# Kernel optimization log

Measured on AMD Instinct MI355X. Metric: run time of the kernel, lower is better.

Reference implementation:

```python
import jax, jax.numpy as jnp
import numpy as np

B, T, N, CIN, C, L, NC, S = 8, 64, 200, 200, 128, 2, 2, 100
SPARSITY = 30


def bn(x, g, b, eps=1e-5):
    # BatchNorm1d forward with batch statistics (training-mode math, biased var)
    m = x.mean(0)
    v = x.var(0)
    return (x - m) / jnp.sqrt(v + eps) * g + b


def ln(x, g, b, eps=1e-5):
    m = x.mean(-1, keepdims=True)
    v = x.var(-1, keepdims=True)
    return (x - m) / jnp.sqrt(v + eps) * g + b


def setup_inputs() -> dict:
    key = jax.random.key(0)
    ks = iter(jax.random.split(key, 64))

    def nrm(shape, s=0.02):
        return jax.random.normal(next(ks), shape, jnp.float32) * s

    return dict(
        fMRI_v=jax.random.normal(next(ks), (B, T, N, CIN), jnp.float32),
        fMRI_a=jax.random.uniform(next(ks), (B, T, N, N), jnp.float32),
        sMRI_trad=jax.random.normal(next(ks), (B, S), jnp.float32),
        sMRI_deep=jnp.zeros((B, 1, 8, 8, 8), jnp.float32),
        csatt=1, CA_MOD=0,
        w_init=nrm((CIN, C)), b_init=jnp.zeros((C,), jnp.float32),
        gin_eps=jnp.zeros((L,), jnp.float32),
        gin_w1=nrm((L, C, C)), gin_b1=jnp.zeros((L, C), jnp.float32),
        gin_bn1_g=jnp.ones((L, C), jnp.float32), gin_bn1_b=jnp.zeros((L, C), jnp.float32),
        gin_w2=nrm((L, C, C)), gin_b2=jnp.zeros((L, C), jnp.float32),
        gin_bn2_g=jnp.ones((L, C), jnp.float32), gin_bn2_b=jnp.zeros((L, C), jnp.float32),
        sero_w=nrm((L, C, C)), sero_b=jnp.zeros((L, C), jnp.float32),
        sero_bn_g=jnp.ones((L, C), jnp.float32), sero_bn_b=jnp.zeros((L, C), jnp.float32),
        sero_aw=nrm((L, C, N)), sero_ab=jnp.zeros((L, N), jnp.float32),
        tr_wqkv=nrm((L, C, 3 * C)), tr_bqkv=jnp.zeros((L, 3 * C), jnp.float32),
        tr_wo=nrm((L, C, C)), tr_bo=jnp.zeros((L, C), jnp.float32),
        tr_ln1_g=jnp.ones((L, C), jnp.float32), tr_ln1_b=jnp.zeros((L, C), jnp.float32),
        tr_ln2_g=jnp.ones((L, C), jnp.float32), tr_ln2_b=jnp.zeros((L, C), jnp.float32),
        tr_w1=nrm((L, C, 2 * C)), tr_b1=jnp.zeros((L, 2 * C), jnp.float32),
        tr_w2=nrm((L, 2 * C, C)), tr_b2=jnp.zeros((L, C), jnp.float32),
        cls_w=nrm((L, C, NC)), cls_b=jnp.zeros((L, NC), jnp.float32),
        smri_w=nrm((S, C)), smri_b=jnp.zeros((C,), jnp.float32),
        smri_bn_g=jnp.ones((C,), jnp.float32), smri_bn_b=jnp.zeros((C,), jnp.float32),
    )


def reference(fMRI_v, fMRI_a, sMRI_trad, sMRI_deep, csatt, CA_MOD,
              w_init, b_init, gin_eps,
              gin_w1, gin_b1, gin_bn1_g, gin_bn1_b,
              gin_w2, gin_b2, gin_bn2_g, gin_bn2_b,
              sero_w, sero_b, sero_bn_g, sero_bn_b, sero_aw, sero_ab,
              tr_wqkv, tr_bqkv, tr_wo, tr_bo,
              tr_ln1_g, tr_ln1_b, tr_ln2_g, tr_ln2_b,
              tr_w1, tr_b1, tr_w2, tr_b2,
              cls_w, cls_b, smri_w, smri_b, smri_bn_g, smri_bn_b):
    b, t, n = fMRI_a.shape[:3]
    # initial linear over flattened (b t n) tokens
    h3 = (fMRI_v.reshape(-1, fMRI_v.shape[-1]) @ w_init + b_init).reshape(b, t, n, -1)
    # _collate_adjacency: per-(sample,timepoint) percentile threshold -> block-diag sparse
    # with all-ones values; equivalent to a batched masked matmul.
    thr = jnp.percentile(fMRI_a, 100 - SPARSITY, axis=(-2, -1), keepdims=True)
    mask = (fMRI_a > thr).astype(h3.dtype)  # [b,t,n,n]

    logit = jnp.zeros((b, cls_w.shape[-1]), h3.dtype)
    latents, node_attns, time_attns = [], [], []
    scale = 1.0 / jnp.sqrt(jnp.asarray(h3.shape[-1], h3.dtype))
    for l in range(L):
        # LayerGIN: note the original feeds h3 (initial features) to EVERY layer
        agg = jnp.einsum('btij,btjc->btic', mask, h3) + gin_eps[l] * h3
        x = agg.reshape(-1, agg.shape[-1])
        x = jax.nn.relu(bn(x @ gin_w1[l] + gin_b1[l], gin_bn1_g[l], gin_bn1_b[l]))
        x = jax.nn.relu(bn(x @ gin_w2[l] + gin_b2[l], gin_bn2_g[l], gin_bn2_b[l]))
        hb = x.reshape(b, t, n, -1).transpose(1, 0, 2, 3)  # (t,b,n,c)
        # ModuleSERO readout (node_axis=2)
        xr = hb.mean(2)  # (t,b,c)
        e = jax.nn.gelu(bn(xr.reshape(t * b, -1) @ sero_w[l] + sero_b[l],
                           sero_bn_g[l], sero_bn_b[l]), approximate=False)
        ga = jax.nn.sigmoid(e @ sero_aw[l] + sero_ab[l]).reshape(t, b, n)
        hr = (hb * ga[..., None]).mean(2)  # (t,b,c)
        node_attns.append(ga.transpose(1, 0, 2))  # (b,t,n)
        # ModuleTransformer (single head, post-LN, no residual before ln1)
        qkv = hr @ tr_wqkv[l] + tr_bqkv[l]
        q, k, v = jnp.split(qkv, 3, axis=-1)
        A = jax.nn.softmax(jnp.einsum('tbc,sbc->bts', q, k) * scale, axis=-1)  # (b,t,t)
        att = jnp.einsum('bts,sbc->tbc', A, v) @ tr_wo[l] + tr_bo[l]
        x1 = ln(att, tr_ln1_g[l], tr_ln1_b[l])
        m = jax.nn.relu(x1 @ tr_w1[l] + tr_b1[l]) @ tr_w2[l] + tr_b2[l]
        x2 = ln(x1 + m, tr_ln2_g[l], tr_ln2_b[l])
        time_attns.append(A)
        lat = x2.sum(0)  # cls_token='sum' over time
        logit = logit + lat @ cls_w[l] + cls_b[l]
        latents.append(lat)
    feat_fMRI = jnp.stack(latents, 1).mean(1)  # (b,c)
    feat_sMRI = bn(sMRI_trad @ smri_w + smri_b, smri_bn_g, smri_bn_b)
    node_attn = jnp.stack(node_attns, 1)  # (b,L,t,n)
    time_attn = jnp.stack(time_attns, 1)  # (b,L,t,t)
    return (logit, feat_fMRI, feat_sMRI, node_attn, time_attn)
```

## Files before the change

### kernel.cpp

```cpp
#include <hip/hip_runtime.h>
#include <math.h>

#define B_   8
#define T_   64
#define N_   200
#define CIN_ 200
#define C_   128
#define L_   2
#define NC_  2
#define S_   100
#define BT_  512
#define RB_  102400

#define ACT_NONE 0
#define ACT_RELU 1
#define ACT_GELU 2

typedef __attribute__((ext_vector_type(8))) short short8v;
typedef __attribute__((ext_vector_type(4))) float f32x4v;

union U4S8 { uint4 u; short8v s; };

__device__ __forceinline__ unsigned short f2bf(float f) {
    unsigned u = __float_as_uint(f);
    unsigned r = (u + 0x7FFFu + ((u >> 16) & 1u)) >> 16;
    return (unsigned short)r;
}
__device__ __forceinline__ float bf2f(unsigned short u) {
    return __uint_as_float(((unsigned)u) << 16);
}
__device__ __forceinline__ float bflo(unsigned u) { return __uint_as_float(u << 16); }
__device__ __forceinline__ float bfhi(unsigned u) { return __uint_as_float(u & 0xFFFF0000u); }
__device__ __forceinline__ unsigned packbf(float a, float b) {
    return (unsigned)f2bf(a) | ((unsigned)f2bf(b) << 16);
}

#define GLL(src, dst) __builtin_amdgcn_global_load_lds( \
    (const __attribute__((address_space(1))) unsigned int*)(src), \
    (__attribute__((address_space(3))) unsigned int*)(dst), 16, 0, 0)

__global__ __launch_bounds__(1024) void thr_kernel(const float* __restrict__ a,
                                                   float* __restrict__ thr,
                                                   unsigned* __restrict__ msk) {
    __shared__ int      hist[1024];
    __shared__ int      red[1024];
    __shared__ unsigned smask[1400];
    __shared__ float    candV[6144];
    __shared__ unsigned short candP[6144];
    __shared__ int      part[256];
    __shared__ int      grp[32];
    __shared__ float    cand2[256];
    __shared__ int      meta[8];
    __shared__ float    s_thr;
    int tid = threadIdx.x, lane = tid & 63;
    int bt = blockIdx.x;
    hist[tid] = 0;
    for (int i = tid; i < 1400; i += 1024) smask[i] = 0u;
    if (tid == 0) { meta[0] = 0; meta[1] = 0; }
    __syncthreads();

    const float4* x4 = (const float4*)(a + (long)bt * 40000);
    int c_lo = 0;
    #pragma unroll 1
    for (int it = 0; it < 10; it++) {
        int i4 = tid + it * 1024;
        unsigned nhi = 0u, ncm = 0u;
        float vv[4] = {0.f, 0.f, 0.f, 0.f};
        if (i4 < 10000) {
            float4 v = x4[i4];
            vv[0] = v.x; vv[1] = v.y; vv[2] = v.z; vv[3] = v.w;
            #pragma unroll
            for (int j = 0; j < 4; j++) {
                float f = vv[j];
                if (f < 0.65f) c_lo++;
                else if (f < 0.75f) ncm |= 1u << j;
                else nhi |= 1u << j;
            }
            if (nhi) {
                int vi = i4 * 4;
                int row = vi / 200, col = vi - row * 200;
                atomicOr(&smask[row * 7 + (col >> 5)], nhi << (col & 31));
            }
        }
        int cnt = __popc(ncm);
        int pfx = cnt;
        #pragma unroll
        for (int d = 1; d < 64; d <<= 1) {
            int t = __shfl_up(pfx, d, 64);
            if (lane >= d) pfx += t;
        }
        int total = __shfl(pfx, 63, 64);
        if (total) {
            int bw = 0;
            if (lane == 63) bw = atomicAdd(&meta[0], total);
            bw = __shfl(bw, 63, 64);
            int p = bw + pfx - cnt;
            #pragma unroll
            for (int j = 0; j < 4; j++) {
                if ((ncm >> j) & 1u) {
                    float f = vv[j];
                    if (p < 6144) { candV[p] = f; candP[p] = (unsigned short)(i4 * 4 + j); }
                    int bin = (int)((f - 0.65f) * 10240.0f);
                    bin = bin < 0 ? 0 : (bin > 1023 ? 1023 : bin);
                    atomicAdd(&hist[bin], 1);
                    p++;
                }
            }
        }
    }
    red[tid] = c_lo;
    __syncthreads();
    for (int off = 512; off; off >>= 1) {
        if (tid < off) red[tid] += red[tid + off];
        __syncthreads();
    }
    int c_lo_tot = red[0];
    if (tid < 256) part[tid] = hist[4*tid] + hist[4*tid+1] + hist[4*tid+2] + hist[4*tid+3];
    __syncthreads();
    if (tid < 32) {
        int s = 0;
        for (int i = 0; i < 8; i++) s += part[8*tid + i];
        grp[tid] = s;
    }
    __syncthreads();
    if (tid == 0) {
        int r = 27999 - c_lo_tot;
        int cum = 0, g = 0;
        while (cum + grp[g] <= r) cum += grp[g++];
        int t = g * 8;
        while (cum + part[t] <= r) cum += part[t++];
        int b = t * 4;
        while (cum + hist[b] <= r) cum += hist[b++];
        meta[2] = b; meta[3] = cum;
        int r1 = r + 1;
        cum = 0; g = 0;
        while (cum + grp[g] <= r1) cum += grp[g++];
        t = g * 8;
        while (cum + part[t] <= r1) cum += part[t++];
        b = t * 4;
        while (cum + hist[b] <= r1) cum += hist[b++];
        meta[4] = b; meta[5] = r;
    }
    __syncthreads();
    int blo = meta[2], base = meta[3], bhi = meta[4], r = meta[5];
    int m = meta[0]; if (m > 6144) m = 6144;
    for (int i = tid; i < m; i += 1024) {
        float v = candV[i];
        int bin = (int)((v - 0.65f) * 10240.0f);
        bin = bin < 0 ? 0 : (bin > 1023 ? 1023 : bin);
        if (bin >= blo && bin <= bhi) {
            int p = atomicAdd(&meta[1], 1);
            if (p < 256) cand2[p] = v;
        }
    }
    __syncthreads();
    if (tid == 0) {
        int m2 = meta[1]; if (m2 > 256) m2 = 256;
        for (int i = 1; i < m2; i++) {
            float key = cand2[i]; int j = i - 1;
            while (j >= 0 && cand2[j] > key) { cand2[j+1] = cand2[j]; j--; }
            cand2[j+1] = key;
        }
        float s1 = cand2[r - base], s2 = cand2[r + 1 - base];
        float tv = s1 * 0.701171875f + s2 * 0.298828125f;
        thr[bt] = tv;
        s_thr = tv;
    }
    __syncthreads();
    float tv = s_thr;
    for (int i = tid; i < m; i += 1024) {
        if (candV[i] > tv) {
            int vi = candP[i];
            int row = vi / 200, col = vi - row * 200;
            atomicOr(&smask[row * 7 + (col >> 5)], 1u << (col & 31));
        }
    }
    __syncthreads();
    for (int i = tid; i < 1400; i += 1024)
        msk[(long)bt * 1400 + i] = smask[i];
}

__global__ void wtcvt_kernel(const float* __restrict__ w, int K, int Kpad,
                             unsigned short* __restrict__ wt) {
    int c = blockIdx.x;
    for (int k = threadIdx.x; k < Kpad; k += 64) {
        float v = (k < K) ? w[(long)k * 128 + c] : 0.f;
        wt[(long)c * Kpad + k] = f2bf(v);
    }
}

template<bool A_BF16, bool BN_IN, bool BIAS_OUT, bool STATS_OUT>
__global__ __launch_bounds__(256) void gemm_direct_kernel(
        const void* __restrict__ xv, int K, int Kstride, int Ksteps,
        const unsigned short* __restrict__ wt, int Kpad,
        const float* __restrict__ bias, const float* __restrict__ statsIn,
        const float* __restrict__ bng, const float* __restrict__ bnb,
        unsigned short* __restrict__ y, float* __restrict__ statsOut) {
    constexpr int ASZ  = A_BF16 ? 8192 : 16384;
    constexpr int BOFF = 2 * ASZ;
    constexpr int NEED = 2 * ASZ + 2 * 8192;
    constexpr int POOL = NEED > 32768 ? NEED : 32768;
    __shared__ unsigned char pool[POOL];
    __shared__ float bnS[128], bnB[128];
    int tid = threadIdx.x;
    if (BN_IN) {
        if (tid < 128) {
            float mm = statsIn[tid] * (1.f / (float)RB_);
            float var = fmaxf(statsIn[128 + tid] * (1.f / (float)RB_) - mm * mm, 0.f);
            float sc = bng[tid] / sqrtf(var + 1e-5f);
            bnS[tid] = sc; bnB[tid] = bnb[tid] - mm * sc;
        }
    }
    int wave = tid >> 6, lane = tid & 63, quad = lane >> 4, m16 = lane & 15;
    long row0g = (long)blockIdx.x * 128;

    auto STAGE = [&](int buf, int ks) {
        #pragma unroll
        for (int j = 0; j < 2; j++) {
            int r = j * 64 + (tid >> 2);
            int c = (tid & 3) ^ ((r >> 1) & 3);
            const char* src = (const char*)wt + (long)r * (Kpad * 2) + ks * 64 + c * 16;
            char* dst = (char*)pool + BOFF + buf * 8192 + j * 4096 + wave * 1024;
            GLL(src, dst);
        }
        if (A_BF16) {
            const char* xb = (const char*)xv;
            #pragma unroll
            for (int j = 0; j < 2; j++) {
                int r = j * 64 + (tid >> 2);
                int c = (tid & 3) ^ ((r >> 1) & 3);
                const char* src = xb + ((row0g + r) * Kstride + ks * 32) * 2 + c * 16;
                char* dst = (char*)pool + buf * ASZ + j * 4096 + wave * 1024;
                GLL(src, dst);
            }
        } else {
            const char* xb = (const char*)xv;
            #pragma unroll
            for (int j = 0; j < 4; j++) {
                int r = j * 32 + (tid >> 3);
                int c = (tid & 7) ^ (r & 7);
                const char* src = xb + ((row0g + r) * Kstride + ks * 32) * 4 + c * 16;
                char* dst = (char*)pool + buf * ASZ + j * 4096 + wave * 1024;
                GLL(src, dst);
            }
        }
    };

    f32x4v acc[2][8];
    #pragma unroll
    for (int i = 0; i < 2; i++)
        #pragma unroll
        for (int j = 0; j < 8; j++) acc[i][j] = (f32x4v){0.f, 0.f, 0.f, 0.f};

    STAGE(0, 0);
    __syncthreads();

    for (int ks = 0; ks < Ksteps; ks++) {
        if (ks + 1 < Ksteps) {
            STAGE((ks + 1) & 1, ks + 1);
            if (A_BF16) asm volatile("s_waitcnt vmcnt(4)" ::: "memory");
            else        asm volatile("s_waitcnt vmcnt(6)" ::: "memory");
        } else {
            asm volatile("s_waitcnt vmcnt(0)" ::: "memory");
        }
        __builtin_amdgcn_s_barrier();
        asm volatile("" ::: "memory");

        const char* Ab = (const char*)pool + (ks & 1) * ASZ;
        const char* Bb = (const char*)pool + BOFF + (ks & 1) * 8192;
        int kf = ks * 32 + quad * 8;
        U4S8 bU[8];
        #pragma unroll
        for (int nt = 0; nt < 8; nt++) {
            int r = nt * 16 + m16;
            int ch = quad ^ ((r >> 1) & 3);
            bU[nt].u = *(const uint4*)(Bb + r * 64 + ch * 16);
        }
        U4S8 aU[2];
        if (A_BF16) {
            #pragma unroll
            for (int mt = 0; mt < 2; mt++) {
                int r = wave * 32 + mt * 16 + m16;
                int ch = quad ^ ((r >> 1) & 3);
                aU[mt].u = *(const uint4*)(Ab + r * 64 + ch * 16);
            }
            if (BN_IN) {
                float4 s0 = *(const float4*)&bnS[kf], s1 = *(const float4*)&bnS[kf + 4];
                float4 b0 = *(const float4*)&bnB[kf], b1 = *(const float4*)&bnB[kf + 4];
                #pragma unroll
                for (int mt = 0; mt < 2; mt++) {
                    uint4 u = aU[mt].u;
                    float f0 = fmaxf(bflo(u.x) * s0.x + b0.x, 0.f);
                    float f1 = fmaxf(bfhi(u.x) * s0.y + b0.y, 0.f);
                    float f2 = fmaxf(bflo(u.y) * s0.z + b0.z, 0.f);
                    float f3 = fmaxf(bfhi(u.y) * s0.w + b0.w, 0.f);
                    float f4 = fmaxf(bflo(u.z) * s1.x + b1.x, 0.f);
                    float f5 = fmaxf(bfhi(u.z) * s1.y + b1.y, 0.f);
                    float f6 = fmaxf(bflo(u.w) * s1.z + b1.z, 0.f);
                    float f7 = fmaxf(bfhi(u.w) * s1.w + b1.w, 0.f);
                    u.x = packbf(f0, f1); u.y = packbf(f2, f3);
                    u.z = packbf(f4, f5); u.w = packbf(f6, f7);
                    aU[mt].u = u;
                }
            }
        } else {
            #pragma unroll
            for (int mt = 0; mt < 2; mt++) {
                int r = wave * 32 + mt * 16 + m16;
                int swz = r & 7;
                const char* base = Ab + r * 128;
                float4 v0 = *(const float4*)(base + ((2 * quad) ^ swz) * 16);
                float4 v1 = *(const float4*)(base + ((2 * quad + 1) ^ swz) * 16);
                uint4 o;
                o.x = packbf(v0.x, v0.y); o.y = packbf(v0.z, v0.w);
                o.z = packbf(v1.x, v1.y); o.w = packbf(v1.z, v1.w);
                aU[mt].u = o;
            }
        }
        #pragma unroll
        for (int nt = 0; nt < 8; nt++) {
            acc[0][nt] = __builtin_amdgcn_mfma_f32_16x16x32_bf16(aU[0].s, bU[nt].s, acc[0][nt], 0, 0, 0);
            acc[1][nt] = __builtin_amdgcn_mfma_f32_16x16x32_bf16(aU[1].s, bU[nt].s, acc[1][nt], 0, 0, 0);
        }
        asm volatile("s_waitcnt lgkmcnt(0)" ::: "memory");
        __builtin_amdgcn_s_barrier();
        asm volatile("" ::: "memory");
    }
    if (!A_BF16 && (K & 31) != 0) {
        int kf = Ksteps * 32 + quad * 8;
        U4S8 bU[8];
        #pragma unroll
        for (int nt = 0; nt < 8; nt++)
            bU[nt].u = *(const uint4*)&wt[(long)(nt * 16 + m16) * Kpad + kf];
        U4S8 aU[2];
        const float* x = (const float*)xv;
        #pragma unroll
        for (int mt = 0; mt < 2; mt++) {
            uint4 o = {0u, 0u, 0u, 0u};
            if (kf + 8 <= K) {
                const float* p = &x[(row0g + wave * 32 + mt * 16 + m16) * Kstride + kf];
                float4 v0 = *(const float4*)p;
// ... 251 lines not shown
    unsigned ONEu = 0x3F80u;

    f32x4v acc[2][8];
    #pragma unroll
    for (int i = 0; i < 2; i++)
        #pragma unroll
        for (int j = 0; j < 8; j++) acc[i][j] = (f32x4v){0.f, 0.f, 0.f, 0.f};

    __syncthreads();

    for (int kc = 0; kc < 7; kc++) {
        if (kc < 4) STAGE((kc + 3) & 3, kc + 3);
        if (kc == 3)      asm volatile("s_waitcnt vmcnt(6)" ::: "memory");
        else if (kc == 4) asm volatile("s_waitcnt vmcnt(4)" ::: "memory");
        else if (kc == 5) asm volatile("s_waitcnt vmcnt(2)" ::: "memory");
        else if (kc == 6) asm volatile("s_waitcnt vmcnt(0)" ::: "memory");
        __builtin_amdgcn_s_barrier();
        asm volatile("" ::: "memory");

        const char* sb = (const char*)&u.stage[kc & 3][0];
        U4S8 bU[8];
        #pragma unroll
        for (int nt = 0; nt < 8; nt++) {
            int r = nt * 16 + m16;
            int q = quad ^ ((r >> 1) & 3);
            bU[nt].u = *(const uint4*)(sb + r * 64 + q * 16);
        }
        U4S8 aU[2];
        #pragma unroll
        for (int mt = 0; mt < 2; mt++) {
            int lr = wave * 32 + mt * 16 + m16;
            unsigned bits = (sbits[lr * 7 + kc] >> (quad * 8)) & 0xFFu;
            unsigned o[4];
            #pragma unroll
            for (int p = 0; p < 4; p++) {
                unsigned lo = ((bits >> (2 * p)) & 1u) ? ONEu : 0u;
                unsigned hi = ((bits >> (2 * p + 1)) & 1u) ? ONEu : 0u;
                o[p] = lo | (hi << 16);
            }
            aU[mt].u = make_uint4(o[0], o[1], o[2], o[3]);
        }
        #pragma unroll
        for (int nt = 0; nt < 8; nt++) {
            acc[0][nt] = __builtin_amdgcn_mfma_f32_16x16x32_bf16(aU[0].s, bU[nt].s, acc[0][nt], 0, 0, 0);
            acc[1][nt] = __builtin_amdgcn_mfma_f32_16x16x32_bf16(aU[1].s, bU[nt].s, acc[1][nt], 0, 0, 0);
        }
        asm volatile("s_waitcnt lgkmcnt(0)" ::: "memory");
        __builtin_amdgcn_s_barrier();
        asm volatile("" ::: "memory");
    }

    #pragma unroll
    for (int nt = 0; nt < 8; nt++) {
        int col = nt * 16 + m16;
        #pragma unroll
        for (int mt = 0; mt < 2; mt++) {
            int lrb = wave * 32 + mt * 16 + quad * 4;
            #pragma unroll
            for (int i = 0; i < 4; i++) {
                int lr = lrb + i;
                u.trans[lr * 128 + (col ^ ((lr & 6) << 2))] = f2bf(acc[mt][nt][i]);
            }
        }
    }
    __syncthreads();

    float eps = geps[l];
    f32x4v acc2[2][8];
    #pragma unroll
    for (int i = 0; i < 2; i++)
        #pragma unroll
        for (int j = 0; j < 8; j++) acc2[i][j] = (f32x4v){0.f, 0.f, 0.f, 0.f};

    for (int ks = 0; ks < 4; ks++) {
        int kf = ks * 32 + quad * 8;
        U4S8 bU[8];
        #pragma unroll
        for (int nt = 0; nt < 8; nt++)
            bU[nt].u = *(const uint4*)&w1t[(long)(nt * 16 + m16) * 128 + kf];
        U4S8 aU[2];
        #pragma unroll
        for (int mt = 0; mt < 2; mt++) {
            int r = wave * 32 + mt * 16 + m16;
            uint4 mu = *(const uint4*)&u.trans[r * 128 + (kf ^ ((r & 6) << 2))];
            int gr = row0 + r;
            uint4 hu = {0u, 0u, 0u, 0u};
            if (gr < N_) hu = *(const uint4*)&h3[((long)bt * N_ + gr) * 128 + kf];
            float f0 = bflo(mu.x) + eps * bflo(hu.x);
            float f1 = bfhi(mu.x) + eps * bfhi(hu.x);
            float f2 = bflo(mu.y) + eps * bflo(hu.y);
            float f3 = bfhi(mu.y) + eps * bfhi(hu.y);
            float f4 = bflo(mu.z) + eps * bflo(hu.z);
            float f5 = bfhi(mu.z) + eps * bfhi(hu.z);
            float f6 = bflo(mu.w) + eps * bflo(hu.w);
            float f7 = bfhi(mu.w) + eps * bfhi(hu.w);
            uint4 o;
            o.x = packbf(f0, f1); o.y = packbf(f2, f3);
            o.z = packbf(f4, f5); o.w = packbf(f6, f7);
            aU[mt].u = o;
        }
        #pragma unroll
        for (int nt = 0; nt < 8; nt++) {
            acc2[0][nt] = __builtin_amdgcn_mfma_f32_16x16x32_bf16(aU[0].s, bU[nt].s, acc2[0][nt], 0, 0, 0);
            acc2[1][nt] = __builtin_amdgcn_mfma_f32_16x16x32_bf16(aU[1].s, bU[nt].s, acc2[1][nt], 0, 0, 0);
        }
    }
    __syncthreads();

    float sAcc[8], qAcc[8];
    #pragma unroll
    for (int nt = 0; nt < 8; nt++) {
        int col = nt * 16 + m16;
        float bv = b1[col];
        float s = 0.f, q = 0.f;
        #pragma unroll
        for (int mt = 0; mt < 2; mt++) {
            int lrb = wave * 32 + mt * 16 + quad * 4;
            #pragma unroll
            for (int i = 0; i < 4; i++) {
                int lr = lrb + i;
                float v = acc2[mt][nt][i] + bv;
                u.trans[lr * 128 + (col ^ ((lr & 6) << 2))] = f2bf(v);
                if (row0 + lr < N_) { s += v; q += v * v; }
            }
        }
        sAcc[nt] = s; qAcc[nt] = q;
    }
    __syncthreads();
    #pragma unroll
    for (int rnd = 0; rnd < 8; rnd++) {
        int row = rnd * 16 + (tid >> 4), ch = tid & 15;
        int gr = row0 + row;
        uint4 v = *(const uint4*)&u.trans[row * 128 + ((ch * 8) ^ ((row & 6) << 2))];
        if (gr < N_)
            *(uint4*)&y[((long)bt * N_ + gr) * 128 + ch * 8] = v;
    }
    __syncthreads();
    #pragma unroll
    for (int nt = 0; nt < 8; nt++) {
        int col = nt * 16 + m16;
        u.red.S[col * 16 + wave * 4 + quad] = sAcc[nt];
        u.red.Q[col * 16 + wave * 4 + quad] = qAcc[nt];
    }
    __syncthreads();
    if (tid < 128) {
        float s = 0.f, q = 0.f;
        #pragma unroll
        for (int j = 0; j < 16; j++) { s += u.red.S[tid * 16 + j]; q += u.red.Q[tid * 16 + j]; }
        atomicAdd(&statsOut[tid], s);
        atomicAdd(&statsOut[128 + tid], q);
    }
}

__global__ __launch_bounds__(256) void xr2_kernel(const unsigned short* __restrict__ raw,
                                                  const float* __restrict__ stats,
                                                  const float* __restrict__ g,
                                                  const float* __restrict__ b,
                                                  float* __restrict__ xr) {
    __shared__ float red[256];
    int tid = threadIdx.x, c = tid & 127, hf = tid >> 7;
    int t = blockIdx.x / B_, bb = blockIdx.x % B_;
    const unsigned short* base = raw + ((long)bb * T_ + t) * N_ * C_;
    float m = stats[c] * (1.f / (float)RB_);
    float var = fmaxf(stats[128 + c] * (1.f / (float)RB_) - m * m, 0.f);
    float sc = g[c] / sqrtf(var + 1e-5f);
    float sh = b[c] - m * sc;
    float s = 0.f;
    for (int n = hf * 100; n < hf * 100 + 100; n++)
        s += fmaxf(fmaf(bf2f(base[n * C_ + c]), sc, sh), 0.f);
    red[tid] = s;
    __syncthreads();
    if (hf == 0)
        xr[(long)blockIdx.x * C_ + c] = (red[c] + red[c + 128]) * (1.f / 200.f);
}

__global__ __launch_bounds__(256) void hr2_kernel(const unsigned short* __restrict__ raw,
                                                  const float* __restrict__ stats,
                                                  const float* __restrict__ g,
                                                  const float* __restrict__ b,
                                                  const float* __restrict__ ga,
                                                  float* __restrict__ hr) {
    __shared__ float sga[N_];
    __shared__ float red[256];
    int tid = threadIdx.x, c = tid & 127, hf = tid >> 7;
    int t = blockIdx.x / B_, bb = blockIdx.x % B_;
    const unsigned short* base = raw + ((long)bb * T_ + t) * N_ * C_;
    for (int i = tid; i < N_; i += 256) sga[i] = ga[(long)blockIdx.x * N_ + i];
    __syncthreads();
    float m = stats[c] * (1.f / (float)RB_);
    float var = fmaxf(stats[128 + c] * (1.f / (float)RB_) - m * m, 0.f);
    float sc = g[c] / sqrtf(var + 1e-5f);
    float sh = b[c] - m * sc;
    float s = 0.f;
    for (int n = hf * 100; n < hf * 100 + 100; n++)
        s = fmaf(fmaxf(fmaf(bf2f(base[n * C_ + c]), sc, sh), 0.f), sga[n], s);
    red[tid] = s;
    __syncthreads();
    if (hf == 0)
        hr[(long)blockIdx.x * C_ + c] = (red[c] + red[c + 128]) * (1.f / 200.f);
}

template<int K, int ROWS, bool STATS>
__global__ void mm_kernel(const float* __restrict__ x, const float* __restrict__ w,
                          const float* __restrict__ bias, float* __restrict__ y,
                          int Cout, int act, float* __restrict__ stats) {
    __shared__ float sx[ROWS * K];
    long r0 = (long)blockIdx.x * ROWS;
    for (int idx = threadIdx.x; idx < ROWS * K; idx += blockDim.x)
        sx[idx] = x[r0 * K + idx];
    __syncthreads();
    int c = threadIdx.x;
    float acc[ROWS];
    #pragma unroll
    for (int i = 0; i < ROWS; i++) acc[i] = 0.f;
    for (int k = 0; k < K; k++) {
        float wv = w[k * Cout + c];
        #pragma unroll
        for (int i = 0; i < ROWS; i++) acc[i] = fmaf(sx[i * K + k], wv, acc[i]);
    }
    float bv = bias ? bias[c] : 0.f;
    float s = 0.f, ss = 0.f;
    for (int i = 0; i < ROWS; i++) {
        float vv = acc[i] + bv;
        if (act == ACT_RELU) vv = fmaxf(vv, 0.f);
        y[(r0 + i) * Cout + c] = vv;
        if (STATS) { s += vv; ss += vv * vv; }
    }
    if (STATS) {
        atomicAdd(&stats[c], s);
        atomicAdd(&stats[C_ + c], ss);
    }
}

__global__ __launch_bounds__(256) void ga_kernel(const float* __restrict__ eRaw,
                          const float* __restrict__ stats,
                          const float* __restrict__ sg, const float* __restrict__ sb,
                          const float* __restrict__ aw, const float* __restrict__ ab,
                          float* __restrict__ ga, float* __restrict__ node_out, int l) {
    __shared__ float sx[4 * C_];
    __shared__ float bnS[C_], bnB[C_];
    int tid = threadIdx.x;
    if (tid < C_) {
        float m = stats[tid] * (1.f / (float)BT_);
        float var = fmaxf(stats[C_ + tid] * (1.f / (float)BT_) - m * m, 0.f);
        float inv = 1.f / sqrtf(var + 1e-5f);
        float sc = inv * sg[tid];
        bnS[tid] = sc;
        bnB[tid] = sb[tid] - m * sc;
    }
    __syncthreads();
    long r0 = (long)blockIdx.x * 4;
    for (int idx = tid; idx < 4 * C_; idx += 256) {
        int col = idx & (C_ - 1);
        float v = eRaw[r0 * C_ + idx] * bnS[col] + bnB[col];
        sx[idx] = 0.5f * v * (1.f + erff(v * 0.70710678118654752f));
    }
    __syncthreads();
    int c = tid;
    if (c < N_) {
        float acc[4] = {0.f, 0.f, 0.f, 0.f};
        for (int k = 0; k < C_; k++) {
            float wv = aw[k * N_ + c];
            #pragma unroll
            for (int i = 0; i < 4; i++) acc[i] = fmaf(sx[i * C_ + k], wv, acc[i]);
        }
        float bv = ab[c];
        for (int i = 0; i < 4; i++) {
            int tb = (int)r0 + i;
            int t = tb / B_, b = tb % B_;
            float v = 1.f / (1.f + expf(-(acc[i] + bv)));
            ga[(long)tb * N_ + c] = v;
            node_out[(((long)b * L_ + l) * T_ + t) * N_ + c] = v;
        }
    }
}

__global__ __launch_bounds__(128) void attnav_kernel(const float* __restrict__ qkv,
                            float* __restrict__ time_out, float* __restrict__ attv, int l) {
    __shared__ float q[C_];
    __shared__ float sa[T_];
    int tid = threadIdx.x;
    int t = blockIdx.x / B_, b = blockIdx.x % B_;
    q[tid] = qkv[((long)t * B_ + b) * 384 + tid];
    __syncthreads();
    if (tid < 64) {
        const float* krow = qkv + ((long)tid * B_ + b) * 384 + C_;
        float s = 0.f;
        for (int c = 0; c < C_; c++) s = fmaf(q[c], krow[c], s);
        s *= 0.08838834764831843f;
        float mx = s;
        #pragma unroll
        for (int off = 32; off; off >>= 1) mx = fmaxf(mx, __shfl_xor(mx, off));
        float e = expf(s - mx), sum = e;
        #pragma unroll
        for (int off = 32; off; off >>= 1) sum += __shfl_xor(sum, off);
        float p = e / sum;
        sa[tid] = p;
        time_out[(((long)b * L_ + l) * T_ + t) * T_ + tid] = p;
    }
    __syncthreads();
    float s2 = 0.f;
    for (int sp = 0; sp < T_; sp++)
        s2 = fmaf(sa[sp], qkv[((long)sp * B_ + b) * 384 + 256 + tid], s2);
    attv[((long)t * B_ + b) * C_ + tid] = s2;
}

__global__ __launch_bounds__(128) void mmln_kernel(const float* __restrict__ x,
                          const float* __restrict__ w, const float* __restrict__ bias,
                          const float* __restrict__ g, const float* __restrict__ bb,
                          float* __restrict__ out) {
    __shared__ float sx[2 * C_];
    __shared__ float red[C_];
    int tid = threadIdx.x;
    long r0 = (long)blockIdx.x * 2;
    sx[tid]       = x[r0 * C_ + tid];
    sx[C_ + tid]  = x[r0 * C_ + C_ + tid];
    __syncthreads();
    float a0 = 0.f, a1 = 0.f;
    for (int k = 0; k < C_; k++) {
        float wv = w[k * C_ + tid];
        a0 = fmaf(sx[k], wv, a0);
        a1 = fmaf(sx[C_ + k], wv, a1);
    }
    float bv = bias[tid];
    float v[2] = {a0 + bv, a1 + bv};
    #pragma unroll 1
    for (int r = 0; r < 2; r++) {
        red[tid] = v[r]; __syncthreads();
        for (int off = 64; off; off >>= 1) { if (tid < off) red[tid] += red[tid + off]; __syncthreads(); }
        float m = red[0] * (1.f / C_); __syncthreads();
        float d = v[r] - m;
        red[tid] = d * d; __syncthreads();
        for (int off = 64; off; off >>= 1) { if (tid < off) red[tid] += red[tid + off]; __syncthreads(); }
        float var = red[0] * (1.f / C_); __syncthreads();
        out[(r0 + r) * C_ + tid] = d * (1.f / sqrtf(var + 1e-5f)) * g[tid] + bb[tid];
    }
}

__global__ __launch_bounds__(256) void ffn_kernel(const float* __restrict__ x1,
                          const float* __restrict__ w1, const float* __restrict__ b1,
                          const float* __restrict__ w2, const float* __restrict__ b2,
                          const float* __restrict__ g, const float* __restrict__ bb,
                          float* __restrict__ out) {
    __shared__ float sx[2 * C_];
    __shared__ float mid[2 * 256];
    __shared__ float red[C_];
    int tid = threadIdx.x;
    long r0 = (long)blockIdx.x * 2;
    sx[tid] = x1[r0 * C_ + tid];
    __syncthreads();
    float a0 = 0.f, a1 = 0.f;
    for (int k = 0; k < C_; k++) {
        float wv = w1[k * 256 + tid];
        a0 = fmaf(sx[k], wv, a0);
        a1 = fmaf(sx[C_ + k], wv, a1);
    }
    float bv = b1[tid];
    mid[tid]       = fmaxf(a0 + bv, 0.f);
    mid[256 + tid] = fmaxf(a1 + bv, 0.f);
    __syncthreads();
    float v[2] = {0.f, 0.f};
    if (tid < C_) {
        float c0 = 0.f, c1 = 0.f;
        for (int k = 0; k < 256; k++) {
            float wv = w2[k * C_ + tid];
            c0 = fmaf(mid[k], wv, c0);
            c1 = fmaf(mid[256 + k], wv, c1);
        }
        float bv2 = b2[tid];
        v[0] = c0 + bv2 + sx[tid];
        v[1] = c1 + bv2 + sx[C_ + tid];
    }
    #pragma unroll 1
    for (int r = 0; r < 2; r++) {
        if (tid < C_) red[tid] = v[r];
        __syncthreads();
        for (int off = 64; off; off >>= 1) { if (tid < off) red[tid] += red[tid + off]; __syncthreads(); }
        float m = red[0] * (1.f / C_); __syncthreads();
        float d = v[r] - m;
        if (tid < C_) red[tid] = d * d;
        __syncthreads();
        for (int off = 64; off; off >>= 1) { if (tid < off) red[tid] += red[tid + off]; __syncthreads(); }
        float var = red[0] * (1.f / C_); __syncthreads();
        if (tid < C_)
            out[(r0 + r) * C_ + tid] = d * (1.f / sqrtf(var + 1e-5f)) * g[tid] + bb[tid];
    }
}

__global__ void latsum_kernel(const float* __restrict__ x2, float* __restrict__ lat) {
    int b = blockIdx.x, c = threadIdx.x;
    float s = 0.f;
    for (int t = 0; t < T_; t++) s += x2[((long)t * B_ + b) * C_ + c];
    lat[(long)b * C_ + c] = s;
}

__global__ void final_kernel(const float* __restrict__ lat, const float* __restrict__ cls_w,
                             const float* __restrict__ cls_b, float* __restrict__ out) {
    int idx = blockIdx.x * blockDim.x + threadIdx.x;
    if (idx < B_ * NC_) {
        int b = idx / NC_, nc = idx % NC_;
        float s = 0.f;
        for (int l = 0; l < L_; l++) {
            float acc = 0.f;
            for (int c = 0; c < C_; c++)
                acc = fmaf(lat[l * B_ * C_ + b * C_ + c], cls_w[l * C_ * NC_ + c * NC_ + nc], acc);
            s += acc + cls_b[l * NC_ + nc];
        }
        out[idx] = s;
    } else if (idx < B_ * NC_ + B_ * C_) {
        int j = idx - B_ * NC_;
        out[idx] = 0.5f * (lat[j] + lat[B_ * C_ + j]);
    }
}

__global__ void smri_kernel(const float* __restrict__ trad, const float* __restrict__ w,
                            const float* __restrict__ bias, const float* __restrict__ g,
                            const float* __restrict__ bb, float* __restrict__ out) {
    int c = threadIdx.x;
    float y[B_];
    for (int b = 0; b < B_; b++) {
        float s = bias[c];
        for (int k = 0; k < S_; k++) s = fmaf(trad[b * S_ + k], w[k * C_ + c], s);
        y[b] = s;
    }
    float m = 0.f;
    for (int b = 0; b < B_; b++) m += y[b];
    m *= (1.f / B_);
    float var = 0.f;
    for (int b = 0; b < B_; b++) { float d = y[b] - m; var += d * d; }
    var *= (1.f / B_);
    float inv = 1.f / sqrtf(var + 1e-5f);
    for (int b = 0; b < B_; b++) out[b * C_ + c] = (y[b] - m) * inv * g[c] + bb[c];
}

extern "C" void kernel_launch(void* const* d_in, const int* in_sizes, int n_in,
                              void* d_out, int out_size, void* d_ws, size_t ws_size,
                              hipStream_t stream) {
    const float* fv       = (const float*)d_in[0];
    const float* fa       = (const float*)d_in[1];
    const float* trad     = (const float*)d_in[2];
    const float* w_init   = (const float*)d_in[6];
    const float* b_init   = (const float*)d_in[7];
    const float* gin_eps  = (const float*)d_in[8];
    const float* gin_w1   = (const float*)d_in[9];
    const float* gin_b1   = (const float*)d_in[10];
    const float* gbn1g    = (const float*)d_in[11];
    const float* gbn1b    = (const float*)d_in[12];
    const float* gin_w2   = (const float*)d_in[13];
    const float* gin_b2   = (const float*)d_in[14];
    const float* gbn2g    = (const float*)d_in[15];
    const float* gbn2b    = (const float*)d_in[16];
    const float* sero_w   = (const float*)d_in[17];
    const float* sero_b   = (const float*)d_in[18];
    const float* sbng     = (const float*)d_in[19];
    const float* sbnb     = (const float*)d_in[20];
    const float* sero_aw  = (const float*)d_in[21];
    const float* sero_ab  = (const float*)d_in[22];
    const float* wqkv     = (const float*)d_in[23];
    const float* bqkv     = (const float*)d_in[24];
    const float* wo       = (const float*)d_in[25];
    const float* bo       = (const float*)d_in[26];
    const float* ln1g     = (const float*)d_in[27];
    const float* ln1b     = (const float*)d_in[28];
    const float* ln2g     = (const float*)d_in[29];
    const float* ln2b     = (const float*)d_in[30];
    const float* tw1      = (const float*)d_in[31];
    const float* tb1      = (const float*)d_in[32];
    const float* tw2      = (const float*)d_in[33];
    const float* tb2      = (const float*)d_in[34];
    const float* cls_w    = (const float*)d_in[35];
    const float* cls_b    = (const float*)d_in[36];
    const float* smri_w   = (const float*)d_in[37];
    const float* smri_b   = (const float*)d_in[38];
    const float* smri_g   = (const float*)d_in[39];
    const float* smri_bb  = (const float*)d_in[40];

    float* out = (float*)d_out;

    const long SZ_BIG = (long)RB_ * C_;
    unsigned short* H3b = (unsigned short*)d_ws;
    unsigned short* Y1b = H3b + SZ_BIG;
    unsigned short* Y2b = Y1b + SZ_BIG;
    unsigned short* ZTb = Y2b + SZ_BIG;
    float* fbase = (float*)(ZTb + (long)BT_ * 128 * 224);
    float* THR  = fbase;
    float* STAT = THR + 512;
    float* XR   = STAT + 256;
    float* E    = XR  + BT_ * C_;
    float* GA   = E   + BT_ * C_;
    float* HR   = GA  + BT_ * N_;
    float* QKV  = HR  + BT_ * C_;
    float* ATTV = QKV + BT_ * 3 * C_;
    float* ATT  = ATTV + BT_ * C_;
    float* X1   = ATT + BT_ * C_;
    float* MMB  = X1  + BT_ * C_;
    float* X2   = MMB + BT_ * 2 * C_;
    float* LAT  = X2  + BT_ * C_;
    float* STATB = MMB;
    unsigned short* WT0 = (unsigned short*)(LAT + L_ * B_ * C_);
    unsigned short* WT1 = WT0 + 128 * 224;
    unsigned short* WT2 = WT1 + 2 * 128 * 128;
    unsigned* MSK = (unsigned*)(WT2 + 2 * 128 * 128);

    float* OUT_LOGIT = out;
    float* OUT_FEATS = out + 1040;
    float* OUT_NODE  = out + 2064;
    float* OUT_TIME  = out + 206864;

    wtcvt_kernel<<<128, 64, 0, stream>>>(w_init, 200, 224, WT0);
    wtcvt_kernel<<<128, 64, 0, stream>>>(gin_w1,           128, 128, WT1);
    wtcvt_kernel<<<128, 64, 0, stream>>>(gin_w1 + C_ * C_, 128, 128, WT1 + 128 * 128);
    wtcvt_kernel<<<128, 64, 0, stream>>>(gin_w2,           128, 128, WT2);
    wtcvt_kernel<<<128, 64, 0, stream>>>(gin_w2 + C_ * C_, 128, 128, WT2 + 128 * 128);

    h3gemmT_kernel<<<RB_ / 128, 256, 0, stream>>>(fv, WT0, b_init, H3b, ZTb);
    thr_kernel<<<BT_, 1024, 0, stream>>>(fa, THR, MSK);

    for (int l = 0; l < L_; l++) {
        hipMemsetAsync(STAT, 0, 256 * sizeof(float), stream);
        maskfused_kernel<<<BT_ * 2, 256, 0, stream>>>(MSK, ZTb, H3b, WT1 + l * 128 * 128,
            gin_eps, l, gin_b1 + l * C_, Y2b, STAT);
        hipMemsetAsync(STATB, 0, 256 * sizeof(float), stream);
        gemm_direct_kernel<true, true, true, true><<<RB_ / 128, 256, 0, stream>>>(
            Y2b, 128, 128, 4, WT2 + l * 128 * 128, 128, gin_b2 + l * C_, STAT,
            gbn1g + l * C_, gbn1b + l * C_, Y1b, STATB);
        xr2_kernel<<<BT_, 256, 0, stream>>>(Y1b, STATB, gbn2g + l * C_, gbn2b + l * C_, XR);

        hipMemsetAsync(STAT, 0, 256 * sizeof(float), stream);
        mm_kernel<128, 2, true><<<BT_ / 2, 128, 0, stream>>>(
            XR, sero_w + l * C_ * C_, sero_b + l * C_, E, C_, ACT_NONE, STAT);
        ga_kernel<<<BT_ / 4, 256, 0, stream>>>(E, STAT, sbng + l * C_, sbnb + l * C_,
            sero_aw + l * C_ * N_, sero_ab + l * N_, GA, OUT_NODE, l);
        hr2_kernel<<<BT_, 256, 0, stream>>>(Y1b, STATB, gbn2g + l * C_, gbn2b + l * C_, GA, HR);

        mm_kernel<128, 2, false><<<BT_ / 2, 384, 0, stream>>>(
            HR, wqkv + l * C_ * 3 * C_, bqkv + l * 3 * C_, QKV, 3 * C_, ACT_NONE, nullptr);
        attnav_kernel<<<BT_, 128, 0, stream>>>(QKV, OUT_TIME, ATTV, l);
        mmln_kernel<<<BT_ / 2, 128, 0, stream>>>(ATTV, wo + l * C_ * C_, bo + l * C_,
            ln1g + l * C_, ln1b + l * C_, X1);
        ffn_kernel<<<BT_ / 2, 256, 0, stream>>>(X1, tw1 + l * C_ * 2 * C_, tb1 + l * 2 * C_,
            tw2 + l * 2 * C_ * C_, tb2 + l * C_, ln2g + l * C_, ln2b + l * C_, X2);
        latsum_kernel<<<B_, 128, 0, stream>>>(X2, LAT + l * B_ * C_);
    }

    final_kernel<<<5, 256, 0, stream>>>(LAT, cls_w, cls_b, OUT_LOGIT);
    smri_kernel<<<1, 128, 0, stream>>>(trad, smri_w, smri_b, smri_g, smri_bb, OUT_FEATS);
}
```

Before: 773.6 us.

## Fuse small tail kernels and batch weight conversion and memsets

Merges the five weight-conversion launches into one kernel and replaces the per-layer stat memsets with a single upfront memset over per-layer stat buffers. Fuses the node-mean reduction with the SERO linear layer, the weighted node-mean with the QKV projection, the attention with the output projection and LayerNorm, and the FFN output with the time-sum via atomics. This cuts launch count and intermediate global traffic in the latency-bound tail. In exchange, some fused matvecs now run with less parallelism per block, and the atomic time-sum gives a nondeterministic summation order.

```diff
diff --git a/kernel.cpp b/kernel.cpp
--- a/kernel.cpp
+++ b/kernel.cpp
@@ -11,10 +11,6 @@
 #define S_   100
 #define BT_  512
 #define RB_  102400
-
-#define ACT_NONE 0
-#define ACT_RELU 1
-#define ACT_GELU 2
 
 typedef __attribute__((ext_vector_type(8))) short short8v;
 typedef __attribute__((ext_vector_type(4))) float f32x4v;
@@ -180,13 +176,19 @@
         msk[(long)bt * 1400 + i] = smask[i];
 }
 
-__global__ void wtcvt_kernel(const float* __restrict__ w, int K, int Kpad,
-                             unsigned short* __restrict__ wt) {
-    int c = blockIdx.x;
-    for (int k = threadIdx.x; k < Kpad; k += 64) {
-        float v = (k < K) ? w[(long)k * 128 + c] : 0.f;
-        wt[(long)c * Kpad + k] = f2bf(v);
-    }
+__global__ void wtcvt5_kernel(const float* __restrict__ w_init,
+                              const float* __restrict__ gin_w1,
+                              const float* __restrict__ gin_w2,
+                              unsigned short* __restrict__ WT0,
+                              unsigned short* __restrict__ WT1,
+                              unsigned short* __restrict__ WT2) {
+    int grp = blockIdx.x >> 7, c = blockIdx.x & 127;
+    const float* w; unsigned short* wt; int K, Kpad;
+    if (grp == 0)      { w = w_init;                     wt = WT0;                     K = 200; Kpad = 224; }
+    else if (grp <= 2) { w = gin_w1 + (grp - 1) * C_ * C_; wt = WT1 + (grp - 1) * 128 * 128; K = 128; Kpad = 128; }
+    else               { w = gin_w2 + (grp - 3) * C_ * C_; wt = WT2 + (grp - 3) * 128 * 128; K = 128; Kpad = 128; }
+    for (int k = threadIdx.x; k < Kpad; k += 64)
+        wt[(long)c * Kpad + k] = f2bf((k < K) ? w[(long)k * 128 + c] : 0.f);
 }
 
 template<bool A_BF16, bool BN_IN, bool BIAS_OUT, bool STATS_OUT>
@@ -744,12 +746,13 @@
     }
 }
 
-__global__ __launch_bounds__(256) void xr2_kernel(const unsigned short* __restrict__ raw,
-                                                  const float* __restrict__ stats,
-                                                  const float* __restrict__ g,
-                                                  const float* __restrict__ b,
-                                                  float* __restrict__ xr) {
+__global__ __launch_bounds__(256) void xrE_kernel(
+        const unsigned short* __restrict__ raw, const float* __restrict__ stats,
+        const float* __restrict__ g, const float* __restrict__ b,
+        const float* __restrict__ sw, const float* __restrict__ sb,
+        float* __restrict__ E, float* __restrict__ statE) {
     __shared__ float red[256];
+    __shared__ float xrrow[128];
     int tid = threadIdx.x, c = tid & 127, hf = tid >> 7;
     int t = blockIdx.x / B_, bb = blockIdx.x % B_;
     const unsigned short* base = raw + ((long)bb * T_ + t) * N_ * C_;
@@ -762,65 +765,18 @@
         s += fmaxf(fmaf(bf2f(base[n * C_ + c]), sc, sh), 0.f);
     red[tid] = s;
     __syncthreads();
-    if (hf == 0)
-        xr[(long)blockIdx.x * C_ + c] = (red[c] + red[c + 128]) * (1.f / 200.f);
-}
-
-__global__ __launch_bounds__(256) void hr2_kernel(const unsigned short* __restrict__ raw,
-                                                  const float* __restrict__ stats,
-                                                  const float* __restrict__ g,
-                                                  const float* __restrict__ b,
-                                                  const float* __restrict__ ga,
-                                                  float* __restrict__ hr) {
-    __shared__ float sga[N_];
-    __shared__ float red[256];
-    int tid = threadIdx.x, c = tid & 127, hf = tid >> 7;
-    int t = blockIdx.x / B_, bb = blockIdx.x % B_;
-    const unsigned short* base = raw + ((long)bb * T_ + t) * N_ * C_;
-    for (int i = tid; i < N_; i += 256) sga[i] = ga[(long)blockIdx.x * N_ + i];
-    __syncthreads();
-    float m = stats[c] * (1.f / (float)RB_);
-    float var = fmaxf(stats[128 + c] * (1.f / (float)RB_) - m * m, 0.f);
-    float sc = g[c] / sqrtf(var + 1e-5f);
-    float sh = b[c] - m * sc;
-    float s = 0.f;
-    for (int n = hf * 100; n < hf * 100 + 100; n++)
-        s = fmaf(fmaxf(fmaf(bf2f(base[n * C_ + c]), sc, sh), 0.f), sga[n], s);
-    red[tid] = s;
-    __syncthreads();
-    if (hf == 0)
-        hr[(long)blockIdx.x * C_ + c] = (red[c] + red[c + 128]) * (1.f / 200.f);
-}
-
-template<int K, int ROWS, bool STATS>
-__global__ void mm_kernel(const float* __restrict__ x, const float* __restrict__ w,
-                          const float* __restrict__ bias, float* __restrict__ y,
-                          int Cout, int act, float* __restrict__ stats) {
-    __shared__ float sx[ROWS * K];
-    long r0 = (long)blockIdx.x * ROWS;
-    for (int idx = threadIdx.x; idx < ROWS * K; idx += blockDim.x)
-        sx[idx] = x[r0 * K + idx];
-    __syncthreads();
-    int c = threadIdx.x;
-    float acc[ROWS];
-    #pragma unroll
-    for (int i = 0; i < ROWS; i++) acc[i] = 0.f;
-    for (int k = 0; k < K; k++) {
-        float wv = w[k * Cout + c];
-        #pragma unroll
-        for (int i = 0; i < ROWS; i++) acc[i] = fmaf(sx[i * K + k], wv, acc[i]);
-    }
-    float bv = bias ? bias[c] : 0.f;
-    float s = 0.f, ss = 0.f;
-    for (int i = 0; i < ROWS; i++) {
-        float vv = acc[i] + bv;
-        if (act == ACT_RELU) vv = fmaxf(vv, 0.f);
-        y[(r0 + i) * Cout + c] = vv;
-        if (STATS) { s += vv; ss += vv * vv; }
-    }
-    if (STATS) {
-        atomicAdd(&stats[c], s);
-        atomicAdd(&stats[C_ + c], ss);
+    if (hf == 0) xrrow[c] = (red[c] + red[c + 128]) * (1.f / 200.f);
+    __syncthreads();
+    float acc = 0.f;
+    for (int k = hf * 64; k < hf * 64 + 64; k++)
+        acc = fmaf(xrrow[k], sw[k * C_ + c], acc);
+    red[tid] = acc;
+    __syncthreads();
+    if (hf == 0) {
+        float v = red[c] + red[c + 128] + sb[c];
+        E[(long)blockIdx.x * C_ + c] = v;
+        atomicAdd(&statE[c], v);
+        atomicAdd(&statE[C_ + c], v * v);
     }
 }
 
@@ -867,10 +823,46 @@
     }
 }
 
-__global__ __launch_bounds__(128) void attnav_kernel(const float* __restrict__ qkv,
-                            float* __restrict__ time_out, float* __restrict__ attv, int l) {
+__global__ __launch_bounds__(256) void hrQKV_kernel(
+        const unsigned short* __restrict__ raw, const float* __restrict__ stats,
+        const float* __restrict__ g, const float* __restrict__ b,
+        const float* __restrict__ ga, const float* __restrict__ wq,
+        const float* __restrict__ bq, float* __restrict__ qkv) {
+    __shared__ float sga[N_];
+    __shared__ float red[256];
+    __shared__ float hrrow[128];
+    int tid = threadIdx.x, c = tid & 127, hf = tid >> 7;
+    int t = blockIdx.x / B_, bb = blockIdx.x % B_;
+    const unsigned short* base = raw + ((long)bb * T_ + t) * N_ * C_;
+    for (int i = tid; i < N_; i += 256) sga[i] = ga[(long)blockIdx.x * N_ + i];
+    __syncthreads();
+    float m = stats[c] * (1.f / (float)RB_);
+    float var = fmaxf(stats[128 + c] * (1.f / (float)RB_) - m * m, 0.f);
+    float sc = g[c] / sqrtf(var + 1e-5f);
+    float sh = b[c] - m * sc;
+    float s = 0.f;
+    for (int n = hf * 100; n < hf * 100 + 100; n++)
+        s = fmaf(fmaxf(fmaf(bf2f(base[n * C_ + c]), sc, sh), 0.f), sga[n], s);
+    red[tid] = s;
+    __syncthreads();
+    if (hf == 0) hrrow[c] = (red[c] + red[c + 128]) * (1.f / 200.f);
+    __syncthreads();
+    for (int out = tid; out < 384; out += 256) {
+        float acc = 0.f;
+        for (int k = 0; k < C_; k++)
+            acc = fmaf(hrrow[k], wq[k * 384 + out], acc);
+        qkv[(long)blockIdx.x * 384 + out] = acc + bq[out];
+    }
+}
+
+__global__ __launch_bounds__(128) void attnln_kernel(const float* __restrict__ qkv,
+        const float* __restrict__ wo, const float* __restrict__ bo,
+        const float* __restrict__ g, const float* __restrict__ bb,
+        float* __restrict__ time_out, float* __restrict__ x1, int l) {
     __shared__ float q[C_];
     __shared__ float sa[T_];
+    __shared__ float av[C_];
+    __shared__ float red[C_];
     int tid = threadIdx.x;
     int t = blockIdx.x / B_, b = blockIdx.x % B_;
     q[tid] = qkv[((long)t * B_ + b) * 384 + tid];
@@ -894,46 +886,26 @@
     float s2 = 0.f;
     for (int sp = 0; sp < T_; sp++)
         s2 = fmaf(sa[sp], qkv[((long)sp * B_ + b) * 384 + 256 + tid], s2);
-    attv[((long)t * B_ + b) * C_ + tid] = s2;
-}
-
-__global__ __launch_bounds__(128) void mmln_kernel(const float* __restrict__ x,
-                          const float* __restrict__ w, const float* __restrict__ bias,
-                          const float* __restrict__ g, const float* __restrict__ bb,
-                          float* __restrict__ out) {
-    __shared__ float sx[2 * C_];
-    __shared__ float red[C_];
-    int tid = threadIdx.x;
-    long r0 = (long)blockIdx.x * 2;
-    sx[tid]       = x[r0 * C_ + tid];
-    sx[C_ + tid]  = x[r0 * C_ + C_ + tid];
-    __syncthreads();
-    float a0 = 0.f, a1 = 0.f;
-    for (int k = 0; k < C_; k++) {
-        float wv = w[k * C_ + tid];
-        a0 = fmaf(sx[k], wv, a0);
-        a1 = fmaf(sx[C_ + k], wv, a1);
-    }
-    float bv = bias[tid];
-    float v[2] = {a0 + bv, a1 + bv};
-    #pragma unroll 1
-    for (int r = 0; r < 2; r++) {
-        red[tid] = v[r]; __syncthreads();
-        for (int off = 64; off; off >>= 1) { if (tid < off) red[tid] += red[tid + off]; __syncthreads(); }
-        float m = red[0] * (1.f / C_); __syncthreads();
-        float d = v[r] - m;
-        red[tid] = d * d; __syncthreads();
-        for (int off = 64; off; off >>= 1) { if (tid < off) red[tid] += red[tid + off]; __syncthreads(); }
-        float var = red[0] * (1.f / C_); __syncthreads();
-        out[(r0 + r) * C_ + tid] = d * (1.f / sqrtf(var + 1e-5f)) * g[tid] + bb[tid];
-    }
+    av[tid] = s2;
+    __syncthreads();
+    float a0 = 0.f;
+    for (int k = 0; k < C_; k++) a0 = fmaf(av[k], wo[k * C_ + tid], a0);
+    float v = a0 + bo[tid];
+    red[tid] = v; __syncthreads();
+    for (int off = 64; off; off >>= 1) { if (tid < off) red[tid] += red[tid + off]; __syncthreads(); }
+    float m = red[0] * (1.f / C_); __syncthreads();
+    float d = v - m;
+    red[tid] = d * d; __syncthreads();
+    for (int off = 64; off; off >>= 1) { if (tid < off) red[tid] += red[tid + off]; __syncthreads(); }
+    float var = red[0] * (1.f / C_);
+    x1[(long)blockIdx.x * C_ + tid] = d * (1.f / sqrtf(var + 1e-5f)) * g[tid] + bb[tid];
 }
 
 __global__ __launch_bounds__(256) void ffn_kernel(const float* __restrict__ x1,
                           const float* __restrict__ w1, const float* __restrict__ b1,
                           const float* __restrict__ w2, const float* __restrict__ b2,
                           const float* __restrict__ g, const float* __restrict__ bb,
-                          float* __restrict__ out) {
+                          float* __restrict__ lat) {
     __shared__ float sx[2 * C_];
     __shared__ float mid[2 * 256];
     __shared__ float red[C_];
@@ -974,16 +946,12 @@
         __syncthreads();
         for (int off = 64; off; off >>= 1) { if (tid < off) red[tid] += red[tid + off]; __syncthreads(); }
         float var = red[0] * (1.f / C_); __syncthreads();
-        if (tid < C_)
-            out[(r0 + r) * C_ + tid] = d * (1.f / sqrtf(var + 1e-5f)) * g[tid] + bb[tid];
-    }
-}
-
-__global__ void latsum_kernel(const float* __restrict__ x2, float* __restrict__ lat) {
-    int b = blockIdx.x, c = threadIdx.x;
-    float s = 0.f;
-    for (int t = 0; t < T_; t++) s += x2[((long)t * B_ + b) * C_ + c];
-    lat[(long)b * C_ + c] = s;
+        if (tid < C_) {
+            float outv = d * (1.f / sqrtf(var + 1e-5f)) * g[tid] + bb[tid];
+            int b = (int)((r0 + r) % B_);
+            atomicAdd(&lat[b * C_ + tid], outv);
+        }
+    }
 }
 
 __global__ void final_kernel(const float* __restrict__ lat, const float* __restrict__ cls_w,
@@ -1076,20 +1044,13 @@
     unsigned short* ZTb = Y2b + SZ_BIG;
     float* fbase = (float*)(ZTb + (long)BT_ * 128 * 224);
     float* THR  = fbase;
-    float* STAT = THR + 512;
-    float* XR   = STAT + 256;
-    float* E    = XR  + BT_ * C_;
-    float* GA   = E   + BT_ * C_;
-    float* HR   = GA  + BT_ * N_;
-    float* QKV  = HR  + BT_ * C_;
-    float* ATTV = QKV + BT_ * 3 * C_;
-    float* ATT  = ATTV + BT_ * C_;
-    float* X1   = ATT + BT_ * C_;
-    float* MMB  = X1  + BT_ * C_;
-    float* X2   = MMB + BT_ * 2 * C_;
-    float* LAT  = X2  + BT_ * C_;
-    float* STATB = MMB;
-    unsigned short* WT0 = (unsigned short*)(LAT + L_ * B_ * C_);
+    float* SBUF = THR + 512;
+    float* LAT  = SBUF + 1536;
+    float* E    = LAT + 2048;
+    float* GA   = E + BT_ * C_;
+    float* QKV  = GA + BT_ * N_;
+    float* X1   = QKV + BT_ * 3 * C_;
+    unsigned short* WT0 = (unsigned short*)(X1 + BT_ * C_);
     unsigned short* WT1 = WT0 + 128 * 224;
     unsigned short* WT2 = WT1 + 2 * 128 * 128;
     unsigned* MSK = (unsigned*)(WT2 + 2 * 128 * 128);
@@ -1099,40 +1060,32 @@
     float* OUT_NODE  = out + 2064;
     float* OUT_TIME  = out + 206864;
 
-    wtcvt_kernel<<<128, 64, 0, stream>>>(w_init, 200, 224, WT0);
-    wtcvt_kernel<<<128, 64, 0, stream>>>(gin_w1,           128, 128, WT1);
-    wtcvt_kernel<<<128, 64, 0, stream>>>(gin_w1 + C_ * C_, 128, 128, WT1 + 128 * 128);
-    wtcvt_kernel<<<128, 64, 0, stream>>>(gin_w2,           128, 128, WT2);
-    wtcvt_kernel<<<128, 64, 0, stream>>>(gin_w2 + C_ * C_, 128, 128, WT2 + 128 * 128);
+    wtcvt5_kernel<<<640, 64, 0, stream>>>(w_init, gin_w1, gin_w2, WT0, WT1, WT2);
+    hipMemsetAsync(SBUF, 0, (1536 + 2048) * sizeof(float), stream);
 
     h3gemmT_kernel<<<RB_ / 128, 256, 0, stream>>>(fv, WT0, b_init, H3b, ZTb);
     thr_kernel<<<BT_, 1024, 0, stream>>>(fa, THR, MSK);
 
     for (int l = 0; l < L_; l++) {
-        hipMemsetAsync(STAT, 0, 256 * sizeof(float), stream);
+        float* SA = SBUF + l * 768;
+        float* SB = SA + 256;
+        float* SE = SA + 512;
         maskfused_kernel<<<BT_ * 2, 256, 0, stream>>>(MSK, ZTb, H3b, WT1 + l * 128 * 128,
-            gin_eps, l, gin_b1 + l * C_, Y2b, STAT);
-        hipMemsetAsync(STATB, 0, 256 * sizeof(float), stream);
+            gin_eps, l, gin_b1 + l * C_, Y2b, SA);
         gemm_direct_kernel<true, true, true, true><<<RB_ / 128, 256, 0, stream>>>(
-            Y2b, 128, 128, 4, WT2 + l * 128 * 128, 128, gin_b2 + l * C_, STAT,
-            gbn1g + l * C_, gbn1b + l * C_, Y1b, STATB);
-        xr2_kernel<<<BT_, 256, 0, stream>>>(Y1b, STATB, gbn2g + l * C_, gbn2b + l * C_, XR);
-
-        hipMemsetAsync(STAT, 0, 256 * sizeof(float), stream);
-        mm_kernel<128, 2, true><<<BT_ / 2, 128, 0, stream>>>(
-            XR, sero_w + l * C_ * C_, sero_b + l * C_, E, C_, ACT_NONE, STAT);
-        ga_kernel<<<BT_ / 4, 256, 0, stream>>>(E, STAT, sbng + l * C_, sbnb + l * C_,
+            Y2b, 128, 128, 4, WT2 + l * 128 * 128, 128, gin_b2 + l * C_, SA,
+            gbn1g + l * C_, gbn1b + l * C_, Y1b, SB);
+        xrE_kernel<<<BT_, 256, 0, stream>>>(Y1b, SB, gbn2g + l * C_, gbn2b + l * C_,
+            sero_w + l * C_ * C_, sero_b + l * C_, E, SE);
+        ga_kernel<<<BT_ / 4, 256, 0, stream>>>(E, SE, sbng + l * C_, sbnb + l * C_,
             sero_aw + l * C_ * N_, sero_ab + l * N_, GA, OUT_NODE, l);
-        hr2_kernel<<<BT_, 256, 0, stream>>>(Y1b, STATB, gbn2g + l * C_, gbn2b + l * C_, GA, HR);
-
-        mm_kernel<128, 2, false><<<BT_ / 2, 384, 0, stream>>>(
-            HR, wqkv + l * C_ * 3 * C_, bqkv + l * 3 * C_, QKV, 3 * C_, ACT_NONE, nullptr);
-        attnav_kernel<<<BT_, 128, 0, stream>>>(QKV, OUT_TIME, ATTV, l);
-        mmln_kernel<<<BT_ / 2, 128, 0, stream>>>(ATTV, wo + l * C_ * C_, bo + l * C_,
-            ln1g + l * C_, ln1b + l * C_, X1);
+        hrQKV_kernel<<<BT_, 256, 0, stream>>>(Y1b, SB, gbn2g + l * C_, gbn2b + l * C_,
+            GA, wqkv + l * C_ * 3 * C_, bqkv + l * 3 * C_, QKV);
+        attnln_kernel<<<BT_, 128, 0, stream>>>(QKV, wo + l * C_ * C_, bo + l * C_,
+            ln1g + l * C_, ln1b + l * C_, OUT_TIME, X1, l);
         ffn_kernel<<<BT_ / 2, 256, 0, stream>>>(X1, tw1 + l * C_ * 2 * C_, tb1 + l * 2 * C_,
-            tw2 + l * 2 * C_ * C_, tb2 + l * C_, ln2g + l * C_, ln2b + l * C_, X2);
-        latsum_kernel<<<B_, 128, 0, stream>>>(X2, LAT + l * B_ * C_);
+            tw2 + l * 2 * C_ * C_, tb2 + l * C_, ln2g + l * C_, ln2b + l * C_,
+            LAT + l * B_ * C_);
     }
 
     final_kernel<<<5, 256, 0, stream>>>(LAT, cls_w, cls_b, OUT_LOGIT);
```

Result: faster. 713.4 us (-7.8%).
